# Optimization experiments

Hardware: AMD Instinct MI355X
Metric: run time of the kernel (lower is better)

Reference implementation:

```python
import jax, jax.numpy as jnp
import numpy as np

D_EMB = 128
N_CLASSES = 10
ITEM_DIM = 64


def _mlp(x, w1, b1, w2, b2):
    # torch nn.GELU default is exact (erf) gelu
    return jax.nn.gelu(x @ w1 + b1, approximate=False) @ w2 + b2


def sparsemax(z, axis=-1):
    """Euclidean projection of logits onto the probability simplex (sparsemax)."""
    n = z.shape[axis]
    z_sorted = -jnp.sort(-z, axis=axis)                      # descending
    ks = jnp.arange(1, n + 1, dtype=z.dtype)
    csum = jnp.cumsum(z_sorted, axis=axis)
    support = (1.0 + ks * z_sorted) > csum                   # broadcast over last axis
    k_z = jnp.sum(support, axis=axis, keepdims=True)         # support size
    csum_k = jnp.take_along_axis(csum, k_z.astype(jnp.int32) - 1, axis=axis)
    tau = (csum_k - 1.0) / k_z.astype(z.dtype)
    return jnp.maximum(z - tau, 0.0)


def setup_inputs() -> dict:
    key = jax.random.key(0)
    ks = jax.random.split(key, 22)
    d = D_EMB

    def lin(k, fan_in, fan_out):
        lim = (1.0 / fan_in) ** 0.5
        kw, kb = jax.random.split(k)
        w = jax.random.uniform(kw, (fan_in, fan_out), jnp.float32, -lim, lim)
        b = jax.random.uniform(kb, (fan_out,), jnp.float32, -lim, lim)
        return w, b

    wx1, bx1 = lin(ks[0], ITEM_DIM, d)
    wx2, bx2 = lin(ks[1], d, d)
    wq1, bq1 = lin(ks[2], 1, d)
    wq2, bq2 = lin(ks[3], d, d)
    wqp, bqp = lin(ks[4], d, d)
    wkp, bkp = lin(ks[5], d, d)
    wvp, bvp = lin(ks[6], d, d)
    wp1, bp1 = lin(ks[7], d, d)
    wp2, bp2 = lin(ks[8], d, N_CLASSES)

    x_items = jax.random.normal(ks[9], (32, 16384, ITEM_DIM), jnp.float32)
    x_query = jax.random.normal(ks[10], (32, 1), jnp.float32)
    return {
        "x_items": x_items, "x_query": x_query,
        "wx1": wx1, "bx1": bx1, "wx2": wx2, "bx2": bx2,
        "wq1": wq1, "bq1": bq1, "wq2": wq2, "bq2": bq2,
        "wqp": wqp, "bqp": bqp, "wkp": wkp, "bkp": bkp,
        "wvp": wvp, "bvp": bvp, "wp1": wp1, "bp1": bp1,
        "wp2": wp2, "bp2": bp2,
    }


def reference(x_items, x_query, wx1, bx1, wx2, bx2, wq1, bq1, wq2, bq2,
              wqp, bqp, wkp, bkp, wvp, bvp, wp1, bp1, wp2, bp2):
    # x_items: [B, N, item_dim]; x_query: [B, 1] -> unsqueeze(-1) -> [B, 1, 1]
    h_items = _mlp(x_items, wx1, bx1, wx2, bx2)              # [B, N, d]
    h_query = _mlp(x_query[..., None], wq1, bq1, wq2, bq2)   # [B, 1, d]
    q = h_query @ wqp + bqp                                   # [B, 1, d]
    k = h_items @ wkp + bkp                                   # [B, N, d]
    v = h_items @ wvp + bvp                                   # [B, N, d]
    scale = k.shape[-1] ** -0.5
    scores = jnp.einsum('bqd,bnd->bqn', q, k) * scale         # [B, 1, N]
    attn = sparsemax(scores, axis=-1)                         # simplex mapping
    z = jnp.einsum('bqn,bnd->bqd', attn, v)[:, 0]             # squeeze(1) -> [B, d]
    return _mlp(z, wp1, bp1, wp2, bp2)                        # [B, n_classes]
```

## Files before the change

kernel.cpp:

```cpp
#include <hip/hip_runtime.h>
#include <hip/hip_bf16.h>
#include <cstdint>

#define BATCH 32
#define NITEMS 16384
#define DEMB 128
#define IDIM 64

typedef short short8 __attribute__((ext_vector_type(8)));
typedef float f32x4 __attribute__((ext_vector_type(4)));

__device__ inline unsigned short f2bf(float f) {
    union { float f; unsigned int u; } v; v.f = f;
    unsigned int u = v.u;
    unsigned int r = (u + 0x7FFFu + ((u >> 16) & 1u)) >> 16;
    return (unsigned short)r;
}
__device__ inline float bf2f(unsigned short h) {
    union { unsigned int u; float f; } v; v.u = ((unsigned int)h) << 16;
    return v.f;
}

__device__ inline float gelu_f(float x) {
    float y = fabsf(x) * 0.70710678118654752f;
    float t = __builtin_amdgcn_rcpf(fmaf(0.3275911f, y, 1.0f));
    float p = fmaf(0.5307027145f, t, -0.7265760135f);
    p = fmaf(p, t, 0.7107068705f);
    p = fmaf(p, t, -0.142248368f);
    p = fmaf(p, t, 0.127414796f);
    p = p * t;
    float e = __builtin_amdgcn_exp2f(x * x * -0.72134752044448171f);
    float q = p * e;
    float phi = (x > 0.f) ? (1.0f - q) : q;
    return x * phi;
}

__global__ __launch_bounds__(128) void k0_prep(
    const float* __restrict__ xq, const float* __restrict__ wq1, const float* __restrict__ bq1,
    const float* __restrict__ wq2, const float* __restrict__ bq2,
    const float* __restrict__ wqp, const float* __restrict__ bqp,
    const float* __restrict__ wkp,
    const float* __restrict__ wx1, const float* __restrict__ wx2,
    float* __restrict__ r_out, unsigned short* __restrict__ w1h, unsigned short* __restrict__ w1l) {
    __shared__ float buf1[128], buf2[128], buf3[128], buf4[128];
    int t = threadIdx.x;
    int blk = blockIdx.x;
    if (blk < BATCH) {
        int b = blk;
        float xqv = xq[b];
        buf1[t] = gelu_f(fmaf(xqv, wq1[t], bq1[t]));
        __syncthreads();
        float acc = bq2[t];
        for (int j = 0; j < 128; j++) acc = fmaf(buf1[j], wq2[j * 128 + t], acc);
        buf2[t] = acc;
        __syncthreads();
        acc = bqp[t];
        for (int j = 0; j < 128; j++) acc = fmaf(buf2[j], wqp[j * 128 + t], acc);
        buf3[t] = acc;
        __syncthreads();
        acc = 0.f;
        for (int i = 0; i < 128; i++) acc = fmaf(wkp[t * 128 + i], buf3[i], acc);
        buf4[t] = acc * 0.08838834764831845f;
        __syncthreads();
        acc = 0.f;
        for (int i = 0; i < 128; i++) acc = fmaf(wx2[t * 128 + i], buf4[i], acc);
        r_out[b * 128 + t] = acc;
    } else {
        for (int idx = t; idx < 64 * 128; idx += 128) {
            int k = idx >> 7, n = idx & 127;
            float v = wx1[idx];
            unsigned short hi = f2bf(v);
            float lo = v - bf2f(hi);
            w1h[n * 64 + k] = hi;
            w1l[n * 64 + k] = f2bf(lo);
        }
    }
}

__global__ __launch_bounds__(256) void k1_items(
    const float* __restrict__ x, const unsigned short* __restrict__ w1h,
    const unsigned short* __restrict__ w1l, const float* __restrict__ bx1,
    const float* __restrict__ r_in, float* __restrict__ scores) {
    __shared__ alignas(16) unsigned short lxh[64 * 72];
    __shared__ alignas(16) unsigned short lxl[64 * 72];
    __shared__ float red[4][64];
    int tid = threadIdx.x;
    int wave = tid >> 6, lane = tid & 63;
    int quad = lane >> 4, l15 = lane & 15;
    int tile = blockIdx.x;
    long item0 = (long)tile * 64;
    int b = tile >> 8;

    short8 wh[2][2], wl[2][2];
    for (int s = 0; s < 2; s++)
        for (int mt = 0; mt < 2; mt++) {
            int off = (wave * 32 + mt * 16 + l15) * 64 + s * 32 + quad * 8;
            wh[s][mt] = *(const short8*)(w1h + off);
            wl[s][mt] = *(const short8*)(w1l + off);
        }
    float bias8[2][4], rv8[2][4];
    for (int mt = 0; mt < 2; mt++)
        for (int rr = 0; rr < 4; rr++) {
            int row = wave * 32 + mt * 16 + quad * 4 + rr;
            bias8[mt][rr] = bx1[row];
            rv8[mt][rr] = r_in[b * 128 + row];
        }

    const float* xg = x + item0 * 64;
    for (int p = 0; p < 4; p++) {
        int idx = tid + p * 256;
        int row = idx >> 4, c4 = (idx & 15) * 4;
        float4 v = *(const float4*)(xg + row * 64 + c4);
        unsigned int ux = __float_as_uint(v.x), uy = __float_as_uint(v.y);
        unsigned int uz = __float_as_uint(v.z), uw = __float_as_uint(v.w);
        unsigned int hi01 = __builtin_amdgcn_perm(uy, ux, 0x07060302u);
        unsigned int hi23 = __builtin_amdgcn_perm(uw, uz, 0x07060302u);
        float lx = v.x - __uint_as_float(ux & 0xFFFF0000u);
        float ly = v.y - __uint_as_float(uy & 0xFFFF0000u);
        float lz = v.z - __uint_as_float(uz & 0xFFFF0000u);
        float lw = v.w - __uint_as_float(uw & 0xFFFF0000u);
        unsigned int lo01 = __builtin_amdgcn_perm(__float_as_uint(ly), __float_as_uint(lx), 0x07060302u);
        unsigned int lo23 = __builtin_amdgcn_perm(__float_as_uint(lw), __float_as_uint(lz), 0x07060302u);
        *(uint2*)(lxh + row * 72 + c4) = make_uint2(hi01, hi23);
        *(uint2*)(lxl + row * 72 + c4) = make_uint2(lo01, lo23);
    }
    __syncthreads();

    f32x4 acc[2][4];
    for (int mt = 0; mt < 2; mt++)
        for (int nt = 0; nt < 4; nt++) {
            f32x4 bi = {bias8[mt][0], bias8[mt][1], bias8[mt][2], bias8[mt][3]};
            acc[mt][nt] = bi;
        }

    for (int s = 0; s < 2; s++) {
        int koff = s * 32 + quad * 8;
        short8 xh[4], xl[4];
        for (int nt = 0; nt < 4; nt++) {
            int rb = (nt * 16 + l15) * 72 + koff;
            xh[nt] = *(const short8*)(lxh + rb);
            xl[nt] = *(const short8*)(lxl + rb);
        }
        for (int mt = 0; mt < 2; mt++)
            for (int nt = 0; nt < 4; nt++) {
                acc[mt][nt] = __builtin_amdgcn_mfma_f32_16x16x32_bf16(wh[s][mt], xl[nt], acc[mt][nt], 0, 0, 0);
                acc[mt][nt] = __builtin_amdgcn_mfma_f32_16x16x32_bf16(wl[s][mt], xh[nt], acc[mt][nt], 0, 0, 0);
                acc[mt][nt] = __builtin_amdgcn_mfma_f32_16x16x32_bf16(wh[s][mt], xh[nt], acc[mt][nt], 0, 0, 0);
            }
    }

    float pr[4] = {0.f, 0.f, 0.f, 0.f};
    for (int mt = 0; mt < 2; mt++)
        for (int nt = 0; nt < 4; nt++)
            for (int rr = 0; rr < 4; rr++) {
                float g = gelu_f(acc[mt][nt][rr]);
                pr[nt] = fmaf(g, rv8[mt][rr], pr[nt]);
            }
    for (int nt = 0; nt < 4; nt++) {
        pr[nt] += __shfl_xor(pr[nt], 16);
        pr[nt] += __shfl_xor(pr[nt], 32);
    }
    if (quad == 0)
        for (int nt = 0; nt < 4; nt++)
            red[wave][nt * 16 + l15] = pr[nt];
    __syncthreads();
    if (tid < 64)
        scores[item0 + tid] = red[0][tid] + red[1][tid] + red[2][tid] + red[3][tid];
}

__global__ __launch_bounds__(1024) void k2_tau(const float* __restrict__ scores,
                                               float* __restrict__ tau_out,
                                               float* __restrict__ u) {
    __shared__ float la[2][16], lc[2][16];
    int b = blockIdx.x, t = threadIdx.x;
    int wid = t >> 6, lane = t & 63;
    const float* s = scores + (size_t)b * NITEMS;
    float z[16];
    for (int i = 0; i < 16; i++) z[i] = s[t + i * 1024];
    float tau = -1e30f;
    for (int it = 0; it < 21; it++) {
        int pb = it & 1;
        float ls = 0.f, ct = 0.f;
        for (int i = 0; i < 16; i++) {
            bool a = z[i] > tau;
            ls += a ? z[i] : 0.f;
            ct += a ? 1.f : 0.f;
        }
        for (int off = 32; off; off >>= 1) {
            ls += __shfl_xor(ls, off);
            ct += __shfl_xor(ct, off);
        }
        if (lane == 0) { la[pb][wid] = ls; lc[pb][wid] = ct; }
        __syncthreads();
        float tls = 0.f, tct = 0.f;
        for (int i = 0; i < 16; i++) { tls += la[pb][i]; tct += lc[pb][i]; }
        float ntau = (tls - 1.0f) / tct;
        if (ntau == tau) break;
        tau = ntau;
    }
    if (t == 0) tau_out[b] = tau;
    if (t < 128) u[b * 128 + t] = 0.f;
}

__global__ __launch_bounds__(256) void k3_support(
    const float* __restrict__ scores, const float* __restrict__ tau_in,
    const float* __restrict__ x,
    const float* __restrict__ wx1, const float* __restrict__ bx1,
    const float* __restrict__ wx2, const float* __restrict__ bx2,
    float* __restrict__ u) {
    __shared__ float red[4][128];
    int blk = blockIdx.x;
    int b = blk >> 5;
    int sub = blk & 31;
    int wave = threadIdx.x >> 6, lane = threadIdx.x & 63;
    int wslot = sub * 4 + wave;
    int base = wslot * 128;
    float tau = tau_in[b];
    int t0 = lane, t1 = lane + 64;
    float bb0 = bx1[t0], bb1 = bx1[t1];
    float cc0 = bx2[t0], cc1 = bx2[t1];
    float u0 = 0.f, u1 = 0.f;
    const float* srow = scores + (size_t)b * NITEMS + base;
    for (int half = 0; half < 2; half++) {
        float sv = srow[half * 64 + lane] - tau;
        unsigned long long mask = __ballot(sv > 0.f);
        while (mask) {
            int src = __ffsll((long long)mask) - 1;
            mask &= mask - 1;
            float wgt = __shfl(sv, src);
            int item = base + half * 64 + src;
            const float* xr = x + ((size_t)b * NITEMS + item) * 64;
            float xv = xr[lane];
            float p0 = bb0, p1 = bb1;
            for (int k = 0; k < 64; k++) {
                float xk = __shfl(xv, k);
                p0 = fmaf(xk, wx1[k * 128 + t0], p0);
                p1 = fmaf(xk, wx1[k * 128 + t1], p1);
            }
            float h0 = gelu_f(p0), h1 = gelu_f(p1);
            float a0 = cc0, a1 = cc1;
            for (int j = 0; j < 64; j++) {
                float hj = __shfl(h0, j);
                a0 = fmaf(hj, wx2[j * 128 + t0], a0);
                a1 = fmaf(hj, wx2[j * 128 + t1], a1);
            }
            for (int j = 0; j < 64; j++) {
                float hj = __shfl(h1, j);
                a0 = fmaf(hj, wx2[(j + 64) * 128 + t0], a0);
                a1 = fmaf(hj, wx2[(j + 64) * 128 + t1], a1);
            }
            u0 = fmaf(wgt, a0, u0);
            u1 = fmaf(wgt, a1, u1);
        }
    }
    red[wave][t0] = u0;
    red[wave][t1] = u1;
    __syncthreads();
    if (threadIdx.x < 128) {
        float s = red[0][threadIdx.x] + red[1][threadIdx.x] +
                  red[2][threadIdx.x] + red[3][threadIdx.x];
        atomicAdd(&u[b * 128 + threadIdx.x], s);
    }
}

__global__ __launch_bounds__(128) void k4_head(
    const float* __restrict__ u, const float* __restrict__ wvp, const float* __restrict__ bvp,
    const float* __restrict__ wp1, const float* __restrict__ bp1,
    const float* __restrict__ wp2, const float* __restrict__ bp2,
    float* __restrict__ out) {
    __shared__ float ub[128], zb[128], tb[128];
    int b = blockIdx.x, t = threadIdx.x;
    ub[t] = u[b * 128 + t];
    __syncthreads();
    float z = bvp[t];
    for (int j = 0; j < 128; j++) z = fmaf(ub[j], wvp[j * 128 + t], z);
    zb[t] = z;
    __syncthreads();
    float h = bp1[t];
    for (int j = 0; j < 128; j++) h = fmaf(zb[j], wp1[j * 128 + t], h);
    tb[t] = gelu_f(h);
    __syncthreads();
    if (t < 10) {
        float o = bp2[t];
        for (int j = 0; j < 128; j++) o = fmaf(tb[j], wp2[j * 10 + t], o);
        out[b * 10 + t] = o;
    }
}

extern "C" void kernel_launch(void* const* d_in, const int* in_sizes, int n_in,
                              void* d_out, int out_size, void* d_ws, size_t ws_size,
                              hipStream_t stream) {
    const float* x_items = (const float*)d_in[0];
    const float* x_query = (const float*)d_in[1];
    const float* wx1 = (const float*)d_in[2];
    const float* bx1 = (const float*)d_in[3];
    const float* wx2 = (const float*)d_in[4];
    const float* bx2 = (const float*)d_in[5];
    const float* wq1 = (const float*)d_in[6];
    const float* bq1 = (const float*)d_in[7];
    const float* wq2 = (const float*)d_in[8];
    const float* bq2 = (const float*)d_in[9];
    const float* wqp = (const float*)d_in[10];
    const float* bqp = (const float*)d_in[11];
    const float* wkp = (const float*)d_in[12];
    const float* wvp = (const float*)d_in[14];
    const float* bvp = (const float*)d_in[15];
    const float* wp1 = (const float*)d_in[16];
    const float* bp1 = (const float*)d_in[17];
    const float* wp2 = (const float*)d_in[18];
    const float* bp2 = (const float*)d_in[19];
    float* out = (float*)d_out;

    char* ws = (char*)d_ws;
    float* r_buf        = (float*)(ws);
    unsigned short* w1h = (unsigned short*)(ws + 16384);
    unsigned short* w1l = (unsigned short*)(ws + 32768);
    float* scores       = (float*)(ws + 49152);
    float* tau          = (float*)(ws + 49152 + 2097152);
    float* u            = (float*)(ws + 49152 + 2097152 + 256);

    k0_prep<<<33, 128, 0, stream>>>(x_query, wq1, bq1, wq2, bq2, wqp, bqp, wkp,
                                    wx1, wx2, r_buf, w1h, w1l);
    k1_items<<<(BATCH * NITEMS) / 64, 256, 0, stream>>>(x_items, w1h, w1l, bx1, r_buf, scores);
    k2_tau<<<BATCH, 1024, 0, stream>>>(scores, tau, u);
    k3_support<<<BATCH * 32, 256, 0, stream>>>(scores, tau, x_items, wx1, bx1, wx2, bx2, u);
    k4_head<<<BATCH, 128, 0, stream>>>(u, wvp, bvp, wp1, bp1, wp2, bp2, out);
}
```

Baseline: 316.9 us.

## Compact sparsemax support list in tau kernel and balance support pass over it

The tau kernel now stream-compacts the support items (index and weight z-tau) into a per-batch list using wave ballots and an atomic counter. The support kernel then strides over that compacted list instead of having each wave scan a fixed 128-item slice of scores. This load-balances the expensive per-item MLP recomputation across all waves and removes rescanning the whole score array. The cost is extra global writes, atomics, a counter reset in the prep kernel, and a nondeterministic item order that changes the floating-point summation order.

After: 327.5 us. 3.4% more time.

```diff
diff --git a/kernel.cpp b/kernel.cpp
--- a/kernel.cpp
+++ b/kernel.cpp
@@ -41,7 +41,8 @@
     const float* __restrict__ wqp, const float* __restrict__ bqp,
     const float* __restrict__ wkp,
     const float* __restrict__ wx1, const float* __restrict__ wx2,
-    float* __restrict__ r_out, unsigned short* __restrict__ w1h, unsigned short* __restrict__ w1l) {
+    float* __restrict__ r_out, unsigned short* __restrict__ w1h, unsigned short* __restrict__ w1l,
+    int* __restrict__ ctr) {
     __shared__ float buf1[128], buf2[128], buf3[128], buf4[128];
     int t = threadIdx.x;
     int blk = blockIdx.x;
@@ -66,6 +67,7 @@
         for (int i = 0; i < 128; i++) acc = fmaf(wx2[t * 128 + i], buf4[i], acc);
         r_out[b * 128 + t] = acc;
     } else {
+        if (t < BATCH) ctr[t] = 0;
         for (int idx = t; idx < 64 * 128; idx += 128) {
             int k = idx >> 7, n = idx & 127;
             float v = wx1[idx];
@@ -170,7 +172,10 @@
 
 __global__ __launch_bounds__(1024) void k2_tau(const float* __restrict__ scores,
                                                float* __restrict__ tau_out,
-                                               float* __restrict__ u) {
+                                               float* __restrict__ u,
+                                               int* __restrict__ ctr,
+                                               int* __restrict__ sidx,
+                                               float* __restrict__ swgt) {
     __shared__ float la[2][16], lc[2][16];
     int b = blockIdx.x, t = threadIdx.x;
     int wid = t >> 6, lane = t & 63;
@@ -200,11 +205,27 @@
     }
     if (t == 0) tau_out[b] = tau;
     if (t < 128) u[b * 128 + t] = 0.f;
+
+    size_t lbase = (size_t)b * NITEMS;
+    for (int i = 0; i < 16; i++) {
+        bool hit = z[i] > tau;
+        unsigned long long m = __ballot(hit);
+        if (m) {
+            int base = 0;
+            if (lane == 0) base = atomicAdd(&ctr[b], (int)__popcll(m));
+            base = __shfl(base, 0);
+            if (hit) {
+                int off = __popcll(m & ((1ULL << lane) - 1ULL));
+                sidx[lbase + base + off] = t + i * 1024;
+                swgt[lbase + base + off] = z[i] - tau;
+            }
+        }
+    }
 }
 
 __global__ __launch_bounds__(256) void k3_support(
-    const float* __restrict__ scores, const float* __restrict__ tau_in,
-    const float* __restrict__ x,
+    const int* __restrict__ ctr, const int* __restrict__ sidx,
+    const float* __restrict__ swgt, const float* __restrict__ x,
     const float* __restrict__ wx1, const float* __restrict__ bx1,
     const float* __restrict__ wx2, const float* __restrict__ bx2,
     float* __restrict__ u) {
@@ -214,44 +235,37 @@
     int sub = blk & 31;
     int wave = threadIdx.x >> 6, lane = threadIdx.x & 63;
     int wslot = sub * 4 + wave;
-    int base = wslot * 128;
-    float tau = tau_in[b];
+    int cnt = ctr[b];
     int t0 = lane, t1 = lane + 64;
     float bb0 = bx1[t0], bb1 = bx1[t1];
     float cc0 = bx2[t0], cc1 = bx2[t1];
     float u0 = 0.f, u1 = 0.f;
-    const float* srow = scores + (size_t)b * NITEMS + base;
-    for (int half = 0; half < 2; half++) {
-        float sv = srow[half * 64 + lane] - tau;
-        unsigned long long mask = __ballot(sv > 0.f);
-        while (mask) {
-            int src = __ffsll((long long)mask) - 1;
-            mask &= mask - 1;
-            float wgt = __shfl(sv, src);
-            int item = base + half * 64 + src;
-            const float* xr = x + ((size_t)b * NITEMS + item) * 64;
-            float xv = xr[lane];
-            float p0 = bb0, p1 = bb1;
-            for (int k = 0; k < 64; k++) {
-                float xk = __shfl(xv, k);
-                p0 = fmaf(xk, wx1[k * 128 + t0], p0);
-                p1 = fmaf(xk, wx1[k * 128 + t1], p1);
-            }
-            float h0 = gelu_f(p0), h1 = gelu_f(p1);
-            float a0 = cc0, a1 = cc1;
-            for (int j = 0; j < 64; j++) {
-                float hj = __shfl(h0, j);
-                a0 = fmaf(hj, wx2[j * 128 + t0], a0);
-                a1 = fmaf(hj, wx2[j * 128 + t1], a1);
-            }
-            for (int j = 0; j < 64; j++) {
-                float hj = __shfl(h1, j);
-                a0 = fmaf(hj, wx2[(j + 64) * 128 + t0], a0);
-                a1 = fmaf(hj, wx2[(j + 64) * 128 + t1], a1);
-            }
-            u0 = fmaf(wgt, a0, u0);
-            u1 = fmaf(wgt, a1, u1);
-        }
+    size_t lbase = (size_t)b * NITEMS;
+    for (int pos = wslot; pos < cnt; pos += 128) {
+        float wgt = swgt[lbase + pos];
+        int item = sidx[lbase + pos];
+        const float* xr = x + ((size_t)b * NITEMS + item) * 64;
+        float xv = xr[lane];
+        float p0 = bb0, p1 = bb1;
+        for (int k = 0; k < 64; k++) {
+            float xk = __shfl(xv, k);
+            p0 = fmaf(xk, wx1[k * 128 + t0], p0);
+            p1 = fmaf(xk, wx1[k * 128 + t1], p1);
+        }
+        float h0 = gelu_f(p0), h1 = gelu_f(p1);
+        float a0 = cc0, a1 = cc1;
+        for (int j = 0; j < 64; j++) {
+            float hj = __shfl(h0, j);
+            a0 = fmaf(hj, wx2[j * 128 + t0], a0);
+            a1 = fmaf(hj, wx2[j * 128 + t1], a1);
+        }
+        for (int j = 0; j < 64; j++) {
+            float hj = __shfl(h1, j);
+            a0 = fmaf(hj, wx2[(j + 64) * 128 + t0], a0);
+            a1 = fmaf(hj, wx2[(j + 64) * 128 + t1], a1);
+        }
+        u0 = fmaf(wgt, a0, u0);
+        u1 = fmaf(wgt, a1, u1);
     }
     red[wave][t0] = u0;
     red[wave][t1] = u1;
@@ -316,13 +330,17 @@
     unsigned short* w1h = (unsigned short*)(ws + 16384);
     unsigned short* w1l = (unsigned short*)(ws + 32768);
     float* scores       = (float*)(ws + 49152);
-    float* tau          = (float*)(ws + 49152 + 2097152);
-    float* u            = (float*)(ws + 49152 + 2097152 + 256);
+    float* tau          = (float*)(ws + 2146304);
+    float* u            = (float*)(ws + 2146560);
+    int*   ctr          = (int*)  (ws + 2162944);
+    int*   sidx         = (int*)  (ws + 2163200);
+    float* swgt         = (float*)(ws + 4260352);
 
     k0_prep<<<33, 128, 0, stream>>>(x_query, wq1, bq1, wq2, bq2, wqp, bqp, wkp,
-                                    wx1, wx2, r_buf, w1h, w1l);
+                                    wx1, wx2, r_buf, w1h, w1l, ctr);
     k1_items<<<(BATCH * NITEMS) / 64, 256, 0, stream>>>(x_items, w1h, w1l, bx1, r_buf, scores);
-    k2_tau<<<BATCH, 1024, 0, stream>>>(scores, tau, u);
-    k3_support<<<BATCH * 32, 256, 0, stream>>>(scores, tau, x_items, wx1, bx1, wx2, bx2, u);
+    k2_tau<<<BATCH, 1024, 0, stream>>>(scores, tau, u, ctr, sidx, swgt);
+    k3_support<<<BATCH * 32, 256, 0, stream>>>(ctr, sidx, swgt, x_items,
+                                               wx1, bx1, wx2, bx2, u);
     k4_head<<<BATCH, 128, 0, stream>>>(u, wvp, bvp, wp1, bp1, wp2, bp2, out);
 }
```
